# Optimization experiments

Measured on AMD Instinct MI355X. Metric: run time of the kernel, lower is better.

## Reference

```python
import jax, jax.numpy as jnp
import numpy as np

N_NODES = 100000
N_EDGES = 800000
FEATURE_DIM = 128
DEPTH = 3


def setup_inputs() -> dict:
    key = jax.random.key(0)
    k1, k2, k3 = jax.random.split(key, 3)
    x = jax.random.normal(k1, (N_NODES, FEATURE_DIM), dtype=jnp.float32)
    edge_index = jax.random.randint(k2, (2, N_EDGES), 0, N_NODES, dtype=jnp.int32)
    W = jax.random.normal(k3, (FEATURE_DIM, FEATURE_DIM), dtype=jnp.float32) * (1.0 / np.sqrt(FEATURE_DIM))
    b = jnp.zeros((FEATURE_DIM,), dtype=jnp.float32)
    return {"x": x, "edge_index": edge_index, "W": W, "b": b}


def reference(x, edge_index, W, b):
    n = x.shape[0]
    # PyG GCNConv default: add self-loops, symmetric normalization
    loop = jnp.arange(n, dtype=edge_index.dtype)
    src = jnp.concatenate([edge_index[0], loop])  # [E+N]
    dst = jnp.concatenate([edge_index[1], loop])  # [E+N]
    ones = jnp.ones(src.shape[0], dtype=x.dtype)
    deg = jax.ops.segment_sum(ones, dst, num_segments=n)  # in-degree incl. self-loop
    dis = jnp.where(deg > 0, jax.lax.rsqrt(deg), 0.0)  # deg^{-1/2}
    norm = (dis[src] * dis[dst])[:, None]  # [E+N, 1]

    # depth iterations share the SAME conv weights (time-invariant)
    for _ in range(DEPTH):
        h = x @ W  # [N, D] linear transform first (PyG order)
        msg = h[src] * norm  # gather + normalize, [E+N, D]
        agg = jax.ops.segment_sum(msg, dst, num_segments=n)  # scatter-add
        x = jax.nn.relu(agg + b)  # bias, NullControl adds 0, dropout_rate=0 is identity
    return x
```

## Files before the change

kernel.cpp:

```cpp
#include <hip/hip_runtime.h>

#define FD 128
#define CAP 64

typedef __attribute__((ext_vector_type(8))) short short8;
typedef __attribute__((ext_vector_type(4))) float floatx4;

__device__ inline unsigned short f2bf(float f) {
  unsigned u = __float_as_uint(f);
  u += 0x7fffu + ((u >> 16) & 1u);
  return (unsigned short)(u >> 16);
}
__device__ inline float lo16f(unsigned v) { return __uint_as_float(v << 16); }
__device__ inline float hi16f(unsigned v) { return __uint_as_float(v & 0xffff0000u); }
__device__ inline int imin(int a, int b) { return a < b ? a : b; }
__device__ inline unsigned umin(unsigned a, unsigned b) { return a < b ? a : b; }

__global__ __launch_bounds__(256) void k_prep(const float* __restrict__ W,
                                              short* __restrict__ whi,
                                              int* __restrict__ cursor, int N,
                                              int zB) {
  int b = blockIdx.x;
  if (b < zB) {
    int i = b * 256 + threadIdx.x;
    if (i < N) cursor[i] = 0;
  } else {
    int idx = (b - zB) * 256 + threadIdx.x;
    int j = idx & 7, lane = (idx >> 3) & 63, kt = (idx >> 9) & 3, ct = idx >> 11;
    int k = kt * 32 + (lane >> 4) * 8 + j;
    int n = ct * 16 + (lane & 15);
    whi[idx] = (short)f2bf(W[k * FD + n]);
  }
}

template <bool ABF16, bool SCALED>
__device__ __forceinline__ void gemm_body(const void* __restrict__ Av,
                                          const short* __restrict__ Wf_hi,
                                          const int* __restrict__ cursor,
                                          unsigned short* __restrict__ H,
                                          int N, int bid) {
  __shared__ short whi[FD * FD];
  int tid = threadIdx.x;
#pragma unroll
  for (int it = 0; it < 8; ++it) {
    int idx = (it * 256 + tid) * 8;
    *(short8*)&whi[idx] = *(const short8*)&Wf_hi[idx];
  }
  __syncthreads();

  int wid = tid >> 6, lane = tid & 63;
  int quad = lane >> 4, m = lane & 15;
  int rbase = bid * 128 + wid * 32;

  short8 ahi[2][4];
#pragma unroll
  for (int t = 0; t < 2; ++t) {
    int arow = rbase + t * 16 + m;
    if (arow >= N) arow = N - 1;
    if (ABF16) {
      const unsigned short* ap = (const unsigned short*)Av + (size_t)arow * FD;
#pragma unroll
      for (int kt = 0; kt < 4; ++kt)
        ahi[t][kt] = *(const short8*)(ap + kt * 32 + quad * 8);
    } else {
      const float* ap = (const float*)Av + (size_t)arow * FD;
#pragma unroll
      for (int kt = 0; kt < 4; ++kt) {
        const float* p = ap + kt * 32 + quad * 8;
        float4 a0 = *(const float4*)p;
        float4 a1 = *(const float4*)(p + 4);
        ahi[t][kt][0] = (short)f2bf(a0.x); ahi[t][kt][1] = (short)f2bf(a0.y);
        ahi[t][kt][2] = (short)f2bf(a0.z); ahi[t][kt][3] = (short)f2bf(a0.w);
        ahi[t][kt][4] = (short)f2bf(a1.x); ahi[t][kt][5] = (short)f2bf(a1.y);
        ahi[t][kt][6] = (short)f2bf(a1.z); ahi[t][kt][7] = (short)f2bf(a1.w);
      }
    }
  }

  float dis0[4], dis1[4];
  if constexpr (SCALED) {
#pragma unroll
    for (int r = 0; r < 4; ++r) {
      int row0 = imin(rbase + quad * 4 + r, N - 1);
      int row1 = imin(rbase + 16 + quad * 4 + r, N - 1);
      dis0[r] = rsqrtf((float)(imin(cursor[row0], CAP) + 1));
      dis1[r] = rsqrtf((float)(imin(cursor[row1], CAP) + 1));
    }
  }

#pragma unroll
  for (int ct = 0; ct < 8; ++ct) {
    floatx4 acc0 = {0.f, 0.f, 0.f, 0.f}, acc1 = {0.f, 0.f, 0.f, 0.f};
#pragma unroll
    for (int kt = 0; kt < 4; ++kt) {
      int fo = (((ct << 2) + kt) * 64 + lane) * 8;
      short8 bhi = *(const short8*)&whi[fo];
      acc0 = __builtin_amdgcn_mfma_f32_16x16x32_bf16(ahi[0][kt], bhi, acc0, 0, 0, 0);
      acc1 = __builtin_amdgcn_mfma_f32_16x16x32_bf16(ahi[1][kt], bhi, acc1, 0, 0, 0);
    }
#pragma unroll
    for (int r = 0; r < 4; ++r) {
      int row0 = rbase + quad * 4 + r;
      int row1 = rbase + 16 + quad * 4 + r;
      if constexpr (SCALED) {
        if (row0 < N) H[(size_t)row0 * FD + ct * 16 + m] = f2bf(acc0[r] * dis0[r]);
        if (row1 < N) H[(size_t)row1 * FD + ct * 16 + m] = f2bf(acc1[r] * dis1[r]);
      } else {
        if (row0 < N) H[(size_t)row0 * FD + ct * 16 + m] = f2bf(acc0[r]);
        if (row1 < N) H[(size_t)row1 * FD + ct * 16 + m] = f2bf(acc1[r]);
      }
    }
  }
}

template <bool ABF16>
__global__ __launch_bounds__(256) void k_gemm(const void* __restrict__ Av,
                                              const short* __restrict__ Wf_hi,
                                              const int* __restrict__ cursor,
                                              unsigned short* __restrict__ H, int N) {
  gemm_body<ABF16, true>(Av, Wf_hi, cursor, H, N, blockIdx.x);
}

__global__ __launch_bounds__(256) void k_fill_gemm(
    const float* __restrict__ x, const short* __restrict__ Wf_hi,
    const int* __restrict__ src, const int* __restrict__ dst,
    int* __restrict__ cursor, int* __restrict__ buck,
    unsigned short* __restrict__ H, int N, int E, int gG) {
  int b = blockIdx.x;
  if (b < gG) {
    gemm_body<false, false>(x, Wf_hi, nullptr, H, N, b);
  } else {
    int e = (b - gG) * 256 + threadIdx.x;
    if (e < E) {
      int d = dst[e], s = src[e];
      int pos = atomicAdd(&cursor[d], 1);
      if (pos < CAP) buck[(size_t)d * CAP + pos] = s;
    }
  }
}

template <bool OUTBF16, bool SRCDIS>
__global__ __launch_bounds__(256) void k_agg(const unsigned int* __restrict__ h,
                                             const int* __restrict__ cursor,
                                             const int* __restrict__ buck,
                                             const float* __restrict__ bias,
                                             void* __restrict__ out, int N) {
  int wid = __builtin_amdgcn_readfirstlane(threadIdx.x >> 6);
  int lane = threadIdx.x & 63;
  int i = blockIdx.x * 4 + wid;
  if (i >= N) return;
  int deg = imin(cursor[i], CAP);
  float disi = rsqrtf((float)(deg + 1));
  unsigned v = h[(size_t)i * 64 + lane];
  float wself = SRCDIS ? disi : 1.f;
  float a0 = wself * lo16f(v), a1 = wself * hi16f(v);
  float b0 = 0.f, b1 = 0.f, c0 = 0.f, c1 = 0.f, d0 = 0.f, d1 = 0.f;

  const int4* bp = (const int4*)(buck + (size_t)i * CAP);
  int niter = (deg + 7) >> 3;
  for (int it = 0; it < niter; ++it) {
    int4 sa = bp[2 * it];
    int4 sb = bp[2 * it + 1];
    int srcs[8] = {sa.x, sa.y, sa.z, sa.w, sb.x, sb.y, sb.z, sb.w};
    unsigned g[8];
    int cs[8];
#pragma unroll
    for (int j = 0; j < 8; ++j) {
      unsigned su = (unsigned)__builtin_amdgcn_readfirstlane(srcs[j]);
      su = umin(su, (unsigned)(N - 1));
      g[j] = h[(size_t)su * 64 + lane];
      if (SRCDIS) cs[j] = cursor[su];
    }
    int done = it * 8;
#pragma unroll
    for (int j = 0; j < 8; ++j) {
      float wj;
      if (SRCDIS) {
        float ds = rsqrtf((float)(imin(cs[j], CAP) + 1));
        wj = (done + j < deg) ? ds : 0.f;
      } else {
        wj = (done + j < deg) ? 1.f : 0.f;
      }
      float l = lo16f(g[j]), hh = hi16f(g[j]);
      if (j == 0 || j == 4) { a0 = fmaf(wj, l, a0); a1 = fmaf(wj, hh, a1); }
      else if (j == 1 || j == 5) { b0 = fmaf(wj, l, b0); b1 = fmaf(wj, hh, b1); }
      else if (j == 2 || j == 6) { c0 = fmaf(wj, l, c0); c1 = fmaf(wj, hh, c1); }
      else { d0 = fmaf(wj, l, d0); d1 = fmaf(wj, hh, d1); }
    }
  }

  float2 bb = ((const float2*)bias)[lane];
  float o0 = fmaxf(fmaf(disi, (a0 + b0) + (c0 + d0), bb.x), 0.f);
  float o1 = fmaxf(fmaf(disi, (a1 + b1) + (c1 + d1), bb.y), 0.f);
  if (OUTBF16) {
    unsigned pk = ((unsigned)f2bf(o1) << 16) | (unsigned)f2bf(o0);
    ((unsigned*)out)[(size_t)i * 64 + lane] = pk;
  } else {
    ((float2*)out)[(size_t)i * 64 + lane] = make_float2(o0, o1);
  }
}


extern "C" void kernel_launch(void* const* d_in, const int* in_sizes, int n_in,
                              void* d_out, int out_size, void* d_ws, size_t ws_size,
                              hipStream_t stream) {
  const float* x = (const float*)d_in[0];
  const int* ei = (const int*)d_in[1];
  const float* Wg = (const float*)d_in[2];
  const float* b = (const float*)d_in[3];
  int N = in_sizes[0] / FD;
  int E = in_sizes[1] / 2;
  const int* src = ei;
  const int* dst = ei + E;

  char* p = (char*)d_ws;
  auto alloc = [&](size_t bytes) {
    void* r = (void*)p;
    p += (bytes + 255) & ~(size_t)255;
    return r;
  };
  int* cursor = (int*)alloc((size_t)N * 4);
  int* buck = (int*)alloc((size_t)N * CAP * 4);
  unsigned short* h = (unsigned short*)alloc((size_t)N * FD * 2);
  unsigned short* xb = (unsigned short*)alloc((size_t)N * FD * 2);
  short* wf_hi = (short*)alloc((size_t)FD * FD * 2);

  int zB = (N + 255) / 256;
  int wB = FD * FD / 256;
  int gG = (N + 127) / 128;
  int gA = (N + 3) / 4;
  int gE = (E + 255) / 256;

  k_prep<<<zB + wB, 256, 0, stream>>>(Wg, wf_hi, cursor, N, zB);
  k_fill_gemm<<<gG + gE, 256, 0, stream>>>(x, wf_hi, src, dst, cursor, buck, h,
                                           N, E, gG);

  k_agg<true, true><<<gA, 256, 0, stream>>>((const unsigned*)h, cursor, buck, b, xb, N);
  k_gemm<true><<<gG, 256, 0, stream>>>(xb, wf_hi, cursor, h, N);
  k_agg<true, false><<<gA, 256, 0, stream>>>((const unsigned*)h, cursor, buck, b, xb, N);
  k_gemm<true><<<gG, 256, 0, stream>>>(xb, wf_hi, cursor, h, N);
  k_agg<false, false><<<gA, 256, 0, stream>>>((const unsigned*)h, cursor, buck, b, d_out, N);
}
```

Before: 296.0 us.

## Slice edge bucketing by destination and precompute per-node degree scales

The fill phase now launches eight blocks per edge chunk. Each block handles only the edges whose destination falls in its slice ((d>>4)&7), which is meant to localize atomic and bucket-write traffic. Edge index loads use nontemporal hints. A new small kernel precomputes deg^{-1/2} per node, so the first aggregation gathers one float per source instead of reading the cursor and recomputing rsqrt. The cost is that dst is read eight times, and there is an extra kernel launch and buffer.

```diff
diff --git a/kernel.cpp b/kernel.cpp
--- a/kernel.cpp
+++ b/kernel.cpp
@@ -2,6 +2,7 @@
 
 #define FD 128
 #define CAP 64
+#define GPAD 784
 
 typedef __attribute__((ext_vector_type(8))) short short8;
 typedef __attribute__((ext_vector_type(4))) float floatx4;
@@ -78,7 +79,7 @@
   }
 
   float dis0[4], dis1[4];
-  if constexpr (SCALED) {
+  if (SCALED) {
 #pragma unroll
     for (int r = 0; r < 4; ++r) {
       int row0 = imin(rbase + quad * 4 + r, N - 1);
@@ -102,13 +103,9 @@
     for (int r = 0; r < 4; ++r) {
       int row0 = rbase + quad * 4 + r;
       int row1 = rbase + 16 + quad * 4 + r;
-      if constexpr (SCALED) {
-        if (row0 < N) H[(size_t)row0 * FD + ct * 16 + m] = f2bf(acc0[r] * dis0[r]);
-        if (row1 < N) H[(size_t)row1 * FD + ct * 16 + m] = f2bf(acc1[r] * dis1[r]);
-      } else {
-        if (row0 < N) H[(size_t)row0 * FD + ct * 16 + m] = f2bf(acc0[r]);
-        if (row1 < N) H[(size_t)row1 * FD + ct * 16 + m] = f2bf(acc1[r]);
-      }
+      float s0 = SCALED ? dis0[r] : 1.f, s1 = SCALED ? dis1[r] : 1.f;
+      if (row0 < N) H[(size_t)row0 * FD + ct * 16 + m] = f2bf(acc0[r] * s0);
+      if (row1 < N) H[(size_t)row1 * FD + ct * 16 + m] = f2bf(acc1[r] * s1);
     }
   }
 }
@@ -121,27 +118,38 @@
   gemm_body<ABF16, true>(Av, Wf_hi, cursor, H, N, blockIdx.x);
 }
 
-__global__ __launch_bounds__(256) void k_fill_gemm(
+__global__ __launch_bounds__(256) void k_fillgemm(
     const float* __restrict__ x, const short* __restrict__ Wf_hi,
     const int* __restrict__ src, const int* __restrict__ dst,
     int* __restrict__ cursor, int* __restrict__ buck,
     unsigned short* __restrict__ H, int N, int E, int gG) {
   int b = blockIdx.x;
-  if (b < gG) {
-    gemm_body<false, false>(x, Wf_hi, nullptr, H, N, b);
+  if (b < GPAD) {
+    if (b < gG) gemm_body<false, false>(x, Wf_hi, nullptr, H, N, b);
   } else {
-    int e = (b - gG) * 256 + threadIdx.x;
+    int slice = b & 7;
+    int e = ((b - GPAD) >> 3) * 256 + threadIdx.x;
     if (e < E) {
-      int d = dst[e], s = src[e];
-      int pos = atomicAdd(&cursor[d], 1);
-      if (pos < CAP) buck[(size_t)d * CAP + pos] = s;
-    }
-  }
+      int d = __builtin_nontemporal_load(&dst[e]);
+      if (((d >> 4) & 7) == slice) {
+        int s = __builtin_nontemporal_load(&src[e]);
+        int pos = atomicAdd(&cursor[d], 1);
+        if (pos < CAP) buck[(size_t)d * CAP + pos] = s;
+      }
+    }
+  }
+}
+
+__global__ __launch_bounds__(256) void k_disv(const int* __restrict__ cursor,
+                                              float* __restrict__ disv, int N) {
+  int i = blockIdx.x * 256 + threadIdx.x;
+  if (i < N) disv[i] = rsqrtf((float)(imin(cursor[i], CAP) + 1));
 }
 
 template <bool OUTBF16, bool SRCDIS>
 __global__ __launch_bounds__(256) void k_agg(const unsigned int* __restrict__ h,
                                              const int* __restrict__ cursor,
+                                             const float* __restrict__ disv,
                                              const int* __restrict__ buck,
                                              const float* __restrict__ bias,
                                              void* __restrict__ out, int N) {
@@ -163,29 +171,24 @@
     int4 sb = bp[2 * it + 1];
     int srcs[8] = {sa.x, sa.y, sa.z, sa.w, sb.x, sb.y, sb.z, sb.w};
     unsigned g[8];
-    int cs[8];
+    float ds[8];
 #pragma unroll
     for (int j = 0; j < 8; ++j) {
       unsigned su = (unsigned)__builtin_amdgcn_readfirstlane(srcs[j]);
       su = umin(su, (unsigned)(N - 1));
       g[j] = h[(size_t)su * 64 + lane];
-      if (SRCDIS) cs[j] = cursor[su];
+      if (SRCDIS) ds[j] = disv[su];
     }
     int done = it * 8;
 #pragma unroll
     for (int j = 0; j < 8; ++j) {
-      float wj;
-      if (SRCDIS) {
-        float ds = rsqrtf((float)(imin(cs[j], CAP) + 1));
-        wj = (done + j < deg) ? ds : 0.f;
-      } else {
-        wj = (done + j < deg) ? 1.f : 0.f;
-      }
+      float wbase = SRCDIS ? ds[j] : 1.f;
+      float w = (done + j < deg) ? wbase : 0.f;
       float l = lo16f(g[j]), hh = hi16f(g[j]);
-      if (j == 0 || j == 4) { a0 = fmaf(wj, l, a0); a1 = fmaf(wj, hh, a1); }
-      else if (j == 1 || j == 5) { b0 = fmaf(wj, l, b0); b1 = fmaf(wj, hh, b1); }
-      else if (j == 2 || j == 6) { c0 = fmaf(wj, l, c0); c1 = fmaf(wj, hh, c1); }
-      else { d0 = fmaf(wj, l, d0); d1 = fmaf(wj, hh, d1); }
+      if (j == 0 || j == 4) { a0 = fmaf(w, l, a0); a1 = fmaf(w, hh, a1); }
+      else if (j == 1 || j == 5) { b0 = fmaf(w, l, b0); b1 = fmaf(w, hh, b1); }
+      else if (j == 2 || j == 6) { c0 = fmaf(w, l, c0); c1 = fmaf(w, hh, c1); }
+      else { d0 = fmaf(w, l, d0); d1 = fmaf(w, hh, d1); }
     }
   }
 
@@ -220,6 +223,7 @@
     return r;
   };
   int* cursor = (int*)alloc((size_t)N * 4);
+  float* disv = (float*)alloc((size_t)N * 4);
   int* buck = (int*)alloc((size_t)N * CAP * 4);
   unsigned short* h = (unsigned short*)alloc((size_t)N * FD * 2);
   unsigned short* xb = (unsigned short*)alloc((size_t)N * FD * 2);
@@ -232,12 +236,16 @@
   int gE = (E + 255) / 256;
 
   k_prep<<<zB + wB, 256, 0, stream>>>(Wg, wf_hi, cursor, N, zB);
-  k_fill_gemm<<<gG + gE, 256, 0, stream>>>(x, wf_hi, src, dst, cursor, buck, h,
-                                           N, E, gG);
-
-  k_agg<true, true><<<gA, 256, 0, stream>>>((const unsigned*)h, cursor, buck, b, xb, N);
+  k_fillgemm<<<GPAD + 8 * gE, 256, 0, stream>>>(x, wf_hi, src, dst, cursor,
+                                                buck, h, N, E, gG);
+  k_disv<<<zB, 256, 0, stream>>>(cursor, disv, N);
+
+  k_agg<true, true><<<gA, 256, 0, stream>>>((const unsigned*)h, cursor, disv,
+                                            buck, b, xb, N);
   k_gemm<true><<<gG, 256, 0, stream>>>(xb, wf_hi, cursor, h, N);
-  k_agg<true, false><<<gA, 256, 0, stream>>>((const unsigned*)h, cursor, buck, b, xb, N);
+  k_agg<true, false><<<gA, 256, 0, stream>>>((const unsigned*)h, cursor, disv,
+                                             buck, b, xb, N);
   k_gemm<true><<<gG, 256, 0, stream>>>(xb, wf_hi, cursor, h, N);
-  k_agg<false, false><<<gA, 256, 0, stream>>>((const unsigned*)h, cursor, buck, b, d_out, N);
-}
+  k_agg<false, false><<<gA, 256, 0, stream>>>((const unsigned*)h, cursor, disv,
+                                              buck, b, d_out, N);
+}
```

After: 326.0 us. 1.1x slower.
